# Optimization experiments

Hardware: AMD Instinct MI355X
Metric: run time of the kernel (lower is better)

## Reference

```python
import jax, jax.numpy as jnp
import numpy as np

B, S, E, H = 4, 2048, 1024, 16
D = E // H  # projection_dim = 64


def setup_inputs() -> dict:
    key = jax.random.key(0)
    ks = jax.random.split(key, 6)
    scale = 1.0 / np.sqrt(E)
    return {
        "inputs": jax.random.normal(ks[0], (B, S, E), dtype=jnp.float32),
        "Wq": jax.random.normal(ks[1], (E, E), dtype=jnp.float32) * scale,
        "bq": jnp.zeros((E,), dtype=jnp.float32),
        "Wk": jax.random.normal(ks[2], (E, E), dtype=jnp.float32) * scale,
        "bk": jnp.zeros((E,), dtype=jnp.float32),
        "Wv": jax.random.normal(ks[3], (E, E), dtype=jnp.float32) * scale,
        "bv": jnp.zeros((E,), dtype=jnp.float32),
        "Wo": jax.random.normal(ks[4], (E, E), dtype=jnp.float32) * scale,
        "bo": jnp.zeros((E,), dtype=jnp.float32),
    }


def _split_heads(x):
    # [B,S,E] -> [B,H,S,D]
    b, s, _ = x.shape
    return x.reshape(b, s, H, D).transpose(0, 2, 1, 3)


def reference(inputs, Wq, bq, Wk, bk, Wv, bv, Wo, bo):
    q = _split_heads(inputs @ Wq + bq)
    k = _split_heads(inputs @ Wk + bk)
    v = _split_heads(inputs @ Wv + bv)
    inv_sqrt_d = jnp.float32(1.0) / jnp.sqrt(jnp.float32(D))
    # scores: [B,H,S,S]
    scores = jnp.einsum("bhqd,bhkd->bhqk", q, k) * inv_sqrt_d
    weights = jax.nn.softmax(scores, axis=-1)
    attn = jnp.einsum("bhqk,bhkd->bhqd", weights, v)  # [B,H,S,D]
    attn = attn.transpose(0, 2, 1, 3).reshape(inputs.shape[0], -1, E)  # [B,S,E]
    return attn @ Wo + bo
```

## Files before the change

kernel.cpp:

```cpp
#include <hip/hip_runtime.h>
#include <hip/hip_bf16.h>


#define S_LEN 2048
#define E_DIM 1024
#define H_NUM 16
#define D_DIM 64
#define M_ROWS 8192
#define NT (S_LEN / 64)

typedef float f32x4 __attribute__((ext_vector_type(4)));
typedef __bf16 b16x8 __attribute__((ext_vector_type(8)));
typedef unsigned short u16x8 __attribute__((ext_vector_type(8)));
typedef unsigned short u16x4 __attribute__((ext_vector_type(4)));
typedef unsigned int u32x4 __attribute__((ext_vector_type(4)));

static __device__ __forceinline__ f32x4 mfma_bf16(b16x8 a, b16x8 b, f32x4 c) {
  return __builtin_amdgcn_mfma_f32_16x16x32_bf16(a, b, c, 0, 0, 0);
}

static __device__ __forceinline__ unsigned short f2b(float f) {
  union { float f; unsigned u; } v;
  v.f = f;
  unsigned r = v.u + 0x7fffu + ((v.u >> 16) & 1u);
  return (unsigned short)(r >> 16);
}

static __device__ __forceinline__ unsigned pack_bf16x2(float a, float b) {
  __hip_bfloat162 h2 = __float22bfloat162_rn(make_float2(a, b));
  union { __hip_bfloat162 h; unsigned u; } p;
  p.h = h2;
  return p.u;
}

static __device__ __forceinline__ void async_ld16(const unsigned short* g,
                                                  const unsigned short* lds) {
  __builtin_amdgcn_global_load_lds(
      (const __attribute__((address_space(1))) void*)g,
      (__attribute__((address_space(3))) void*)lds, 16, 0, 0);
}


__global__ __launch_bounds__(256) void f32_to_bf16_kernel(
    const float* __restrict__ in, unsigned short* __restrict__ out, int n4) {
  const int i = blockIdx.x * 256 + threadIdx.x;
  if (i >= n4) return;
  const f32x4 v = *(const f32x4*)&in[(size_t)i * 4];
  u16x4 o;
  o.x = f2b(v.x); o.y = f2b(v.y); o.z = f2b(v.z); o.w = f2b(v.w);
  *(u16x4*)&out[(size_t)i * 4] = o;
}

__global__ __launch_bounds__(256) void transpose_w_kernel(
    const float* __restrict__ in, unsigned short* __restrict__ out) {
  __shared__ float tile[32][33];
  const int bx = blockIdx.x * 32, by = blockIdx.y * 32;
  const int tx = threadIdx.x & 31;
  const int ty = (threadIdx.x >> 5) * 4;
#pragma unroll
  for (int i = 0; i < 4; ++i)
    tile[ty + i][tx] = in[(size_t)(by + ty + i) * 1024 + bx + tx];
  __syncthreads();
#pragma unroll
  for (int i = 0; i < 4; ++i)
    out[(size_t)(bx + ty + i) * 1024 + by + tx] = f2b(tile[tx][ty + i]);
}


template <int OUT_F32>
__global__ __launch_bounds__(256) void gemm_bt_kernel(
    const unsigned short* __restrict__ A, const unsigned short* __restrict__ Bt,
    const float* __restrict__ bias, void* __restrict__ Cout, int M, int N,
    int K, float scale) {
  __shared__ __align__(16) unsigned short As[128 * 32];
  __shared__ __align__(16) unsigned short Bs[128 * 32];

  const int tid = threadIdx.x;
  const int wid = tid >> 6;
  const int l = tid & 63;
  const int g = l >> 4;
  const int c = l & 15;
  const int wm = wid >> 1;
  const int wn = wid & 1;
  const int mbase = blockIdx.x * 128;
  const int nbase = blockIdx.y * 128;
  const int lrow = l >> 2;
  const int scol = (l & 3) * 8;

  f32x4 acc[4][4];
#pragma unroll
  for (int i = 0; i < 4; ++i)
#pragma unroll
    for (int j = 0; j < 4; ++j) acc[i][j] = (f32x4){0.f, 0.f, 0.f, 0.f};

  for (int kt = 0; kt < K; kt += 32) {
#pragma unroll
    for (int i = 0; i < 2; ++i) {
      const int ci = wid * 2 + i;
      const int row = ci * 16 + lrow;
      async_ld16(A + (size_t)(mbase + row) * K + kt + scol, As + ci * 512);
      async_ld16(Bt + (size_t)(nbase + row) * K + kt + scol, Bs + ci * 512);
    }
    __syncthreads();

    b16x8 af[4], bfr[4];
#pragma unroll
    for (int mi = 0; mi < 4; ++mi)
      af[mi] = *(const b16x8*)&As[(wm * 64 + mi * 16 + c) * 32 + g * 8];
#pragma unroll
    for (int ni = 0; ni < 4; ++ni)
      bfr[ni] = *(const b16x8*)&Bs[(wn * 64 + ni * 16 + c) * 32 + g * 8];
#pragma unroll
    for (int mi = 0; mi < 4; ++mi)
#pragma unroll
      for (int ni = 0; ni < 4; ++ni)
        acc[mi][ni] = mfma_bf16(af[mi], bfr[ni], acc[mi][ni]);
    __syncthreads();
  }

#pragma unroll
  for (int ni = 0; ni < 4; ++ni) {
    const int col = nbase + wn * 64 + ni * 16 + c;
    const float bv = bias[col];
#pragma unroll
    for (int mi = 0; mi < 4; ++mi)
#pragma unroll
      for (int r = 0; r < 4; ++r) {
        const int row = mbase + wm * 64 + mi * 16 + g * 4 + r;
        const float v = (acc[mi][ni][r] + bv) * scale;
        if (OUT_F32)
          ((float*)Cout)[(size_t)row * N + col] = v;
        else
          ((unsigned short*)Cout)[(size_t)row * N + col] = f2b(v);
      }
  }
}


__global__ __launch_bounds__(256) void attn_kernel(
    const unsigned short* __restrict__ Q, const unsigned short* __restrict__ K,
    const unsigned short* __restrict__ V, unsigned short* __restrict__ O) {
  __shared__ __align__(16) unsigned short Klds[64 * 72];
  __shared__ __align__(16) unsigned short Vt[64 * 72];

  const int tid = threadIdx.x;
  const int w = tid >> 6;
  const int l = tid & 63;
  const int g = l >> 4;
  const int c = l & 15;
  const int b = blockIdx.y >> 4;
  const int h = blockIdx.y & 15;
  const int qbase = blockIdx.x * 128;
  const size_t base_bh = (size_t)b * S_LEN * E_DIM + h * D_DIM;

  const int srow0 = tid >> 3;
  const int scolc = (tid & 7) * 8;
  const int schunk = scolc >> 3;

  b16x8 qf[2][2];
#pragma unroll
  for (int m = 0; m < 2; ++m)
#pragma unroll
    for (int kk = 0; kk < 2; ++kk) {
      const int row = qbase + w * 32 + m * 16 + c;
      qf[m][kk] = *(const b16x8*)&Q[base_bh + (size_t)row * E_DIM + kk * 32 + g * 8];
    }

  f32x4 o[2][4];
#pragma unroll
  for (int m = 0; m < 2; ++m)
#pragma unroll
    for (int nd = 0; nd < 4; ++nd) o[m][nd] = (f32x4){0.f, 0.f, 0.f, 0.f};
  float mrun[2], lrun[2];
  mrun[0] = mrun[1] = -3.0e38f;
  lrun[0] = lrun[1] = 0.f;

  u16x8 kreg[2], vreg[2];

#define LOAD_TILE(T)                                                        \
  {                                                                         \
    const int kvb_ = (T) * 64;                                              \
    _Pragma("unroll") for (int i = 0; i < 2; ++i) {                         \
      const int row_ = srow0 + i * 32;                                      \
      const size_t ga_ = base_bh + (size_t)(kvb_ + row_) * E_DIM + scolc;   \
      kreg[i] = *(const u16x8*)&K[ga_];                                     \
      vreg[i] = *(const u16x8*)&V[ga_];                                     \
    }                                                                       \
  }
#define WRITE_TILE()                                                        \
  {                                                                         \
    _Pragma("unroll") for (int i = 0; i < 2; ++i) {                         \
      const int row_ = srow0 + i * 32;                                      \
      *(u16x8*)&Klds[row_ * 72 + scolc] = kreg[i];                          \
      const int chunk_ = ((row_ >> 3) ^ schunk) & 7;                        \
      _Pragma("unroll") for (int j = 0; j < 8; ++j)                         \
          Vt[(scolc + j) * 72 + chunk_ * 8 + (row_ & 7)] = vreg[i][j];      \
    }                                                                       \
  }

  LOAD_TILE(0);
  WRITE_TILE();

  const int srcA = (((2 * g) & 3) << 4) + c;
  const int srcB = (((2 * g + 1) & 3) << 4) + c;
  const int fsel = g >> 1;

  for (int t = 0; t < NT; ++t) {
    if (t + 1 < NT) LOAD_TILE(t + 1);
    __syncthreads();

    f32x4 sacc[4][2];
#pragma unroll
    for (int n = 0; n < 4; ++n)
#pragma unroll
      for (int m = 0; m < 2; ++m) sacc[n][m] = (f32x4){0.f, 0.f, 0.f, 0.f};
#pragma unroll
    for (int n = 0; n < 4; ++n)
#pragma unroll
      for (int kk = 0; kk < 2; ++kk) {
        const b16x8 kf = *(const b16x8*)&Klds[(n * 16 + c) * 72 + kk * 32 + g * 8];
#pragma unroll
        for (int m = 0; m < 2; ++m)
          sacc[n][m] = mfma_bf16(kf, qf[m][kk], sacc[n][m]);
      }

#pragma unroll
    for (int m = 0; m < 2; ++m) {
      float mx = sacc[0][m][0];
#pragma unroll
      for (int n = 0; n < 4; ++n)
#pragma unroll
        for (int r = 0; r < 4; ++r) mx = fmaxf(mx, sacc[n][m][r]);
      mx = fmaxf(mx, __shfl_xor(mx, 16));
      mx = fmaxf(mx, __shfl_xor(mx, 32));
      const float mnew = fmaxf(mrun[m], mx);
      const float corr = __expf(mrun[m] - mnew);
      mrun[m] = mnew;
      float ps = 0.f;
#pragma unroll
      for (int n = 0; n < 4; ++n)
#pragma unroll
        for (int r = 0; r < 4; ++r) {
          const float p = __expf(sacc[n][m][r] - mnew);
          sacc[n][m][r] = p;
          ps += p;
        }
      ps += __shfl_xor(ps, 16);
      ps += __shfl_xor(ps, 32);
      lrun[m] = lrun[m] * corr + ps;

#pragma unroll
      for (int r = 0; r < 4; ++r) {
        const float cr = __shfl(corr, g * 20 + r);
#pragma unroll
        for (int nd = 0; nd < 4; ++nd) o[m][nd][r] *= cr;
      }

      unsigned wpk[4][2];
#pragma unroll
      for (int n = 0; n < 4; ++n)
#pragma unroll
        for (int rr = 0; rr < 2; ++rr)
          wpk[n][rr] = pack_bf16x2(sacc[n][m][2 * rr], sacc[n][m][2 * rr + 1]);

#pragma unroll
      for (int kk = 0; kk < 2; ++kk) {
        const unsigned aL0 = (unsigned)__shfl((int)wpk[2 * kk][0], srcA);
        const unsigned aL1 = (unsigned)__shfl((int)wpk[2 * kk][1], srcA);
        const unsigned bL0 = (unsigned)__shfl((int)wpk[2 * kk + 1][0], srcA);
        const unsigned bL1 = (unsigned)__shfl((int)wpk[2 * kk + 1][1], srcA);
        const unsigned aH0 = (unsigned)__shfl((int)wpk[2 * kk][0], srcB);
        const unsigned aH1 = (unsigned)__shfl((int)wpk[2 * kk][1], srcB);
        const unsigned bH0 = (unsigned)__shfl((int)wpk[2 * kk + 1][0], srcB);
        const unsigned bH1 = (unsigned)__shfl((int)wpk[2 * kk + 1][1], srcB);
        union { u32x4 u; b16x8 bv; } pun;
        pun.u = (u32x4){fsel ? bL0 : aL0, fsel ? bL1 : aL1,
                        fsel ? bH0 : aH0, fsel ? bH1 : aH1};
        const b16x8 pf = pun.bv;
#pragma unroll
        for (int nd = 0; nd < 4; ++nd) {
          const int d = nd * 16 + c;
          const int chunk = ((kk * 4 + g) ^ (d >> 3)) & 7;
          const b16x8 vf = *(const b16x8*)&Vt[d * 72 + chunk * 8];
          o[m][nd] = mfma_bf16(pf, vf, o[m][nd]);
        }
      }
    }

    __syncthreads();
    if (t + 1 < NT) WRITE_TILE();
  }

#pragma unroll
  for (int m = 0; m < 2; ++m) {
    const float inv = 1.f / lrun[m];
#pragma unroll
    for (int r = 0; r < 4; ++r) {
      const float ivr = __shfl(inv, g * 20 + r);
      const int row = qbase + w * 32 + m * 16 + g * 4 + r;
#pragma unroll
      for (int nd = 0; nd < 4; ++nd)
        O[base_bh + (size_t)row * E_DIM + nd * 16 + c] = f2b(o[m][nd][r] * ivr);
    }
  }
#undef LOAD_TILE
#undef WRITE_TILE
}


extern "C" void kernel_launch(void* const* d_in, const int* in_sizes, int n_in,
                              void* d_out, int out_size, void* d_ws,
                              size_t ws_size, hipStream_t stream) {
  const float* X = (const float*)d_in[0];
  const float* Wq = (const float*)d_in[1];
  const float* bq = (const float*)d_in[2];
  const float* Wk = (const float*)d_in[3];
  const float* bk = (const float*)d_in[4];
  const float* Wv = (const float*)d_in[5];
  const float* bv = (const float*)d_in[6];
  const float* Wo = (const float*)d_in[7];
  const float* bo = (const float*)d_in[8];
  float* out = (float*)d_out;

  unsigned short* ws = (unsigned short*)d_ws;
  unsigned short* Xb = ws;
  unsigned short* Wqt = Xb + 8388608;
  unsigned short* Wkt = Wqt + 1048576;
  unsigned short* Wvt = Wkt + 1048576;
  unsigned short* Wot = Wvt + 1048576;
  unsigned short* Qb = Wot + 1048576;
  unsigned short* Kb = Qb + 8388608;
  unsigned short* Vb = Kb + 8388608;
  unsigned short* Ab = Xb;

  f32_to_bf16_kernel<<<8192, 256, 0, stream>>>(X, Xb, 2097152);
  dim3 tg(32, 32);
  transpose_w_kernel<<<tg, 256, 0, stream>>>(Wq, Wqt);
  transpose_w_kernel<<<tg, 256, 0, stream>>>(Wk, Wkt);
  transpose_w_kernel<<<tg, 256, 0, stream>>>(Wv, Wvt);
  transpose_w_kernel<<<tg, 256, 0, stream>>>(Wo, Wot);

  dim3 gg(M_ROWS / 128, E_DIM / 128);
  gemm_bt_kernel<0><<<gg, 256, 0, stream>>>(Xb, Wqt, bq, (void*)Qb, M_ROWS,
                                            E_DIM, E_DIM, 0.125f);
  gemm_bt_kernel<0><<<gg, 256, 0, stream>>>(Xb, Wkt, bk, (void*)Kb, M_ROWS,
                                            E_DIM, E_DIM, 1.0f);
  gemm_bt_kernel<0><<<gg, 256, 0, stream>>>(Xb, Wvt, bv, (void*)Vb, M_ROWS,
                                            E_DIM, E_DIM, 1.0f);

  dim3 ga(S_LEN / 128, 4 * H_NUM);
  attn_kernel<<<ga, 256, 0, stream>>>(Qb, Kb, Vb, Ab);

  gemm_bt_kernel<1><<<gg, 256, 0, stream>>>(Ab, Wot, bo, (void*)out, M_ROWS,
                                            E_DIM, E_DIM, 1.0f);
}
```

Baseline: 408.1 us.

## Fuse QKV projections into one GEMM and double-buffer attention K/V tiles

The three Q/K/V projection GEMMs become a single GEMM against the concatenated transposed weights (Wqt/Wkt/Wvt sit contiguously in the workspace), writing an interleaved [M,3072] bf16 buffer that attention reads with stride 3072. This cuts launches and re-reads of X. The attention kernel gets double-buffered K/V LDS tiles, so each iteration needs one barrier instead of two. It also raises wave priority around the MFMA blocks and reorders the P·V loop so each V fragment is shared across both row groups. The price is double the LDS per block and strided QKV reads in attention.

```diff
diff --git a/kernel.cpp b/kernel.cpp
--- a/kernel.cpp
+++ b/kernel.cpp
@@ -8,6 +8,7 @@
 #define D_DIM 64
 #define M_ROWS 8192
 #define NT (S_LEN / 64)
+#define QKV_LD 3072
 
 typedef float f32x4 __attribute__((ext_vector_type(4)));
 typedef __bf16 b16x8 __attribute__((ext_vector_type(8)));
@@ -67,11 +68,10 @@
 }
 
 
-template <int OUT_F32>
-__global__ __launch_bounds__(256) void gemm_bt_kernel(
+__global__ __launch_bounds__(256) void gemm_bt_f32_kernel(
     const unsigned short* __restrict__ A, const unsigned short* __restrict__ Bt,
-    const float* __restrict__ bias, void* __restrict__ Cout, int M, int N,
-    int K, float scale) {
+    const float* __restrict__ bias, float* __restrict__ Cout, int M, int N,
+    int K) {
   __shared__ __align__(16) unsigned short As[128 * 32];
   __shared__ __align__(16) unsigned short Bs[128 * 32];
 
@@ -127,21 +127,83 @@
 #pragma unroll
       for (int r = 0; r < 4; ++r) {
         const int row = mbase + wm * 64 + mi * 16 + g * 4 + r;
-        const float v = (acc[mi][ni][r] + bv) * scale;
-        if (OUT_F32)
-          ((float*)Cout)[(size_t)row * N + col] = v;
-        else
-          ((unsigned short*)Cout)[(size_t)row * N + col] = f2b(v);
+        Cout[(size_t)row * N + col] = acc[mi][ni][r] + bv;
+      }
+  }
+}
+
+__global__ __launch_bounds__(256) void gemm_qkv_kernel(
+    const unsigned short* __restrict__ A, const unsigned short* __restrict__ Bt,
+    const float* __restrict__ bq, const float* __restrict__ bk,
+    const float* __restrict__ bv, unsigned short* __restrict__ Cout) {
+  const int M = M_ROWS, N = QKV_LD, K = E_DIM;
+  __shared__ __align__(16) unsigned short As[128 * 32];
+  __shared__ __align__(16) unsigned short Bs[128 * 32];
+
+  const int tid = threadIdx.x;
+  const int wid = tid >> 6;
+  const int l = tid & 63;
+  const int g = l >> 4;
+  const int c = l & 15;
+  const int wm = wid >> 1;
+  const int wn = wid & 1;
+  const int mbase = blockIdx.x * 128;
+  const int nbase = blockIdx.y * 128;
+  const int lrow = l >> 2;
+  const int scol = (l & 3) * 8;
+
+  f32x4 acc[4][4];
+#pragma unroll
+  for (int i = 0; i < 4; ++i)
+#pragma unroll
+    for (int j = 0; j < 4; ++j) acc[i][j] = (f32x4){0.f, 0.f, 0.f, 0.f};
+
+  for (int kt = 0; kt < K; kt += 32) {
+#pragma unroll
+    for (int i = 0; i < 2; ++i) {
+      const int ci = wid * 2 + i;
+      const int row = ci * 16 + lrow;
+      async_ld16(A + (size_t)(mbase + row) * K + kt + scol, As + ci * 512);
+      async_ld16(Bt + (size_t)(nbase + row) * K + kt + scol, Bs + ci * 512);
+    }
+    __syncthreads();
+
+    b16x8 af[4], bfr[4];
+#pragma unroll
+    for (int mi = 0; mi < 4; ++mi)
+      af[mi] = *(const b16x8*)&As[(wm * 64 + mi * 16 + c) * 32 + g * 8];
+#pragma unroll
+    for (int ni = 0; ni < 4; ++ni)
+      bfr[ni] = *(const b16x8*)&Bs[(wn * 64 + ni * 16 + c) * 32 + g * 8];
+#pragma unroll
+    for (int mi = 0; mi < 4; ++mi)
+#pragma unroll
+      for (int ni = 0; ni < 4; ++ni)
+        acc[mi][ni] = mfma_bf16(af[mi], bfr[ni], acc[mi][ni]);
+    __syncthreads();
+  }
+
+#pragma unroll
+  for (int ni = 0; ni < 4; ++ni) {
+    const int col = nbase + wn * 64 + ni * 16 + c;
+    const float* bp = (col < 1024) ? bq : ((col < 2048) ? bk : bv);
+    const float bvv = bp[col & 1023];
+    const float scale = (col < 1024) ? 0.125f : 1.0f;
+#pragma unroll
+    for (int mi = 0; mi < 4; ++mi)
+#pragma unroll
+      for (int r = 0; r < 4; ++r) {
+        const int row = mbase + wm * 64 + mi * 16 + g * 4 + r;
+        Cout[(size_t)row * N + col] = f2b((acc[mi][ni][r] + bvv) * scale);
       }
   }
 }
 
 
 __global__ __launch_bounds__(256) void attn_kernel(
-    const unsigned short* __restrict__ Q, const unsigned short* __restrict__ K,
-    const unsigned short* __restrict__ V, unsigned short* __restrict__ O) {
-  __shared__ __align__(16) unsigned short Klds[64 * 72];
-  __shared__ __align__(16) unsigned short Vt[64 * 72];
+    const unsigned short* __restrict__ QKV, unsigned short* __restrict__ O) {
+  __shared__ __align__(16) unsigned short Klds[2][64 * 72];
+  __shared__ __align__(16) unsigned short Vt[2][64 * 72];
 
   const int tid = threadIdx.x;
   const int w = tid >> 6;
@@ -151,7 +213,10 @@
   const int b = blockIdx.y >> 4;
   const int h = blockIdx.y & 15;
   const int qbase = blockIdx.x * 128;
-  const size_t base_bh = (size_t)b * S_LEN * E_DIM + h * D_DIM;
+  const size_t base_bh = (size_t)b * S_LEN * QKV_LD + h * D_DIM;
+  const unsigned short* Q = QKV;
+  const unsigned short* K = QKV + 1024;
+  const unsigned short* V = QKV + 2048;
 
   const int srow0 = tid >> 3;
   const int scolc = (tid & 7) * 8;
@@ -163,7 +228,8 @@
 #pragma unroll
     for (int kk = 0; kk < 2; ++kk) {
       const int row = qbase + w * 32 + m * 16 + c;
-      qf[m][kk] = *(const b16x8*)&Q[base_bh + (size_t)row * E_DIM + kk * 32 + g * 8];
+      qf[m][kk] =
+          *(const b16x8*)&Q[base_bh + (size_t)row * QKV_LD + kk * 32 + g * 8];
     }
 
   f32x4 o[2][4];
@@ -177,52 +243,59 @@
 
   u16x8 kreg[2], vreg[2];
 
-#define LOAD_TILE(T)                                                        \
-  {                                                                         \
-    const int kvb_ = (T) * 64;                                              \
-    _Pragma("unroll") for (int i = 0; i < 2; ++i) {                         \
-      const int row_ = srow0 + i * 32;                                      \
-      const size_t ga_ = base_bh + (size_t)(kvb_ + row_) * E_DIM + scolc;   \
-      kreg[i] = *(const u16x8*)&K[ga_];                                     \
-      vreg[i] = *(const u16x8*)&V[ga_];                                     \
-    }                                                                       \
-  }
-#define WRITE_TILE()                                                        \
-  {                                                                         \
-    _Pragma("unroll") for (int i = 0; i < 2; ++i) {                         \
-      const int row_ = srow0 + i * 32;                                      \
-      *(u16x8*)&Klds[row_ * 72 + scolc] = kreg[i];                          \
-      const int chunk_ = ((row_ >> 3) ^ schunk) & 7;                        \
-      _Pragma("unroll") for (int j = 0; j < 8; ++j)                         \
-          Vt[(scolc + j) * 72 + chunk_ * 8 + (row_ & 7)] = vreg[i][j];      \
-    }                                                                       \
+#define LOAD_TILE(T)                                                         \
+  {                                                                          \
+    const int kvb_ = (T) * 64;                                               \
+    _Pragma("unroll") for (int i = 0; i < 2; ++i) {                          \
+      const int row_ = srow0 + i * 32;                                       \
+      const size_t ga_ = base_bh + (size_t)(kvb_ + row_) * QKV_LD + scolc;   \
+      kreg[i] = *(const u16x8*)&K[ga_];                                      \
+      vreg[i] = *(const u16x8*)&V[ga_];                                      \
+    }                                                                        \
+  }
+#define WRITE_TILE(BUF)                                                      \
+  {                                                                          \
+    _Pragma("unroll") for (int i = 0; i < 2; ++i) {                          \
+      const int row_ = srow0 + i * 32;                                       \
+      *(u16x8*)&Klds[BUF][row_ * 72 + scolc] = kreg[i];                      \
+      const int chunk_ = ((row_ >> 3) ^ schunk) & 7;                         \
+      _Pragma("unroll") for (int j = 0; j < 8; ++j)                          \
+          Vt[BUF][(scolc + j) * 72 + chunk_ * 8 + (row_ & 7)] = vreg[i][j];  \
+    }                                                                        \
   }
 
   LOAD_TILE(0);
-  WRITE_TILE();
+  WRITE_TILE(0);
 
   const int srcA = (((2 * g) & 3) << 4) + c;
   const int srcB = (((2 * g + 1) & 3) << 4) + c;
   const int fsel = g >> 1;
 
   for (int t = 0; t < NT; ++t) {
+    const int cur = t & 1;
+    __syncthreads();
+
     if (t + 1 < NT) LOAD_TILE(t + 1);
-    __syncthreads();
 
     f32x4 sacc[4][2];
 #pragma unroll
     for (int n = 0; n < 4; ++n)
 #pragma unroll
       for (int m = 0; m < 2; ++m) sacc[n][m] = (f32x4){0.f, 0.f, 0.f, 0.f};
+    __builtin_amdgcn_s_setprio(1);
 #pragma unroll
     for (int n = 0; n < 4; ++n)
 #pragma unroll
       for (int kk = 0; kk < 2; ++kk) {
-        const b16x8 kf = *(const b16x8*)&Klds[(n * 16 + c) * 72 + kk * 32 + g * 8];
+        const b16x8 kf =
+            *(const b16x8*)&Klds[cur][(n * 16 + c) * 72 + kk * 32 + g * 8];
 #pragma unroll
         for (int m = 0; m < 2; ++m)
           sacc[n][m] = mfma_bf16(kf, qf[m][kk], sacc[n][m]);
       }
+    __builtin_amdgcn_s_setprio(0);
+
+    if (t + 1 < NT) WRITE_TILE(cur ^ 1);
 
 #pragma unroll
     for (int m = 0; m < 2; ++m) {
@@ -248,47 +321,49 @@
       ps += __shfl_xor(ps, 16);
       ps += __shfl_xor(ps, 32);
       lrun[m] = lrun[m] * corr + ps;
-
 #pragma unroll
       for (int r = 0; r < 4; ++r) {
         const float cr = __shfl(corr, g * 20 + r);
 #pragma unroll
         for (int nd = 0; nd < 4; ++nd) o[m][nd][r] *= cr;
       }
-
-      unsigned wpk[4][2];
-#pragma unroll
-      for (int n = 0; n < 4; ++n)
-#pragma unroll
-        for (int rr = 0; rr < 2; ++rr)
-          wpk[n][rr] = pack_bf16x2(sacc[n][m][2 * rr], sacc[n][m][2 * rr + 1]);
-
-#pragma unroll
-      for (int kk = 0; kk < 2; ++kk) {
-        const unsigned aL0 = (unsigned)__shfl((int)wpk[2 * kk][0], srcA);
-        const unsigned aL1 = (unsigned)__shfl((int)wpk[2 * kk][1], srcA);
-        const unsigned bL0 = (unsigned)__shfl((int)wpk[2 * kk + 1][0], srcA);
-        const unsigned bL1 = (unsigned)__shfl((int)wpk[2 * kk + 1][1], srcA);
-        const unsigned aH0 = (unsigned)__shfl((int)wpk[2 * kk][0], srcB);
-        const unsigned aH1 = (unsigned)__shfl((int)wpk[2 * kk][1], srcB);
-        const unsigned bH0 = (unsigned)__shfl((int)wpk[2 * kk + 1][0], srcB);
-        const unsigned bH1 = (unsigned)__shfl((int)wpk[2 * kk + 1][1], srcB);
+    }
+
+#pragma unroll
+    for (int kk = 0; kk < 2; ++kk) {
+      b16x8 pf[2];
+#pragma unroll
+      for (int m = 0; m < 2; ++m) {
+        const unsigned w00 = pack_bf16x2(sacc[2 * kk][m][0], sacc[2 * kk][m][1]);
+        const unsigned w01 = pack_bf16x2(sacc[2 * kk][m][2], sacc[2 * kk][m][3]);
+        const unsigned w10 =
+            pack_bf16x2(sacc[2 * kk + 1][m][0], sacc[2 * kk + 1][m][1]);
+        const unsigned w11 =
+            pack_bf16x2(sacc[2 * kk + 1][m][2], sacc[2 * kk + 1][m][3]);
+        const unsigned aL0 = (unsigned)__shfl((int)w00, srcA);
+        const unsigned aL1 = (unsigned)__shfl((int)w01, srcA);
+        const unsigned bL0 = (unsigned)__shfl((int)w10, srcA);
+        const unsigned bL1 = (unsigned)__shfl((int)w11, srcA);
+        const unsigned aH0 = (unsigned)__shfl((int)w00, srcB);
+        const unsigned aH1 = (unsigned)__shfl((int)w01, srcB);
+        const unsigned bH0 = (unsigned)__shfl((int)w10, srcB);
+        const unsigned bH1 = (unsigned)__shfl((int)w11, srcB);
         union { u32x4 u; b16x8 bv; } pun;
         pun.u = (u32x4){fsel ? bL0 : aL0, fsel ? bL1 : aL1,
                         fsel ? bH0 : aH0, fsel ? bH1 : aH1};
-        const b16x8 pf = pun.bv;
-#pragma unroll
-        for (int nd = 0; nd < 4; ++nd) {
-          const int d = nd * 16 + c;
-          const int chunk = ((kk * 4 + g) ^ (d >> 3)) & 7;
-          const b16x8 vf = *(const b16x8*)&Vt[d * 72 + chunk * 8];
-          o[m][nd] = mfma_bf16(pf, vf, o[m][nd]);
-        }
-      }
-    }
-
-    __syncthreads();
-    if (t + 1 < NT) WRITE_TILE();
+        pf[m] = pun.bv;
+      }
+      __builtin_amdgcn_s_setprio(1);
+#pragma unroll
+      for (int nd = 0; nd < 4; ++nd) {
+        const int d = nd * 16 + c;
+        const int chunk = ((kk * 4 + g) ^ (d >> 3)) & 7;
+        const b16x8 vf = *(const b16x8*)&Vt[cur][d * 72 + chunk * 8];
+        o[0][nd] = mfma_bf16(pf[0], vf, o[0][nd]);
+        o[1][nd] = mfma_bf16(pf[1], vf, o[1][nd]);
+      }
+      __builtin_amdgcn_s_setprio(0);
+    }
   }
 
 #pragma unroll
@@ -298,9 +373,10 @@
     for (int r = 0; r < 4; ++r) {
       const float ivr = __shfl(inv, g * 20 + r);
       const int row = qbase + w * 32 + m * 16 + g * 4 + r;
+      const size_t obase = (size_t)b * S_LEN * E_DIM + h * D_DIM;
 #pragma unroll
       for (int nd = 0; nd < 4; ++nd)
-        O[base_bh + (size_t)row * E_DIM + nd * 16 + c] = f2b(o[m][nd][r] * ivr);
+        O[obase + (size_t)row * E_DIM + nd * 16 + c] = f2b(o[m][nd][r] * ivr);
     }
   }
 #undef LOAD_TILE
@@ -328,9 +404,7 @@
   unsigned short* Wkt = Wqt + 1048576;
   unsigned short* Wvt = Wkt + 1048576;
   unsigned short* Wot = Wvt + 1048576;
-  unsigned short* Qb = Wot + 1048576;
-  unsigned short* Kb = Qb + 8388608;
-  unsigned short* Vb = Kb + 8388608;
+  unsigned short* QKVb = Wot + 1048576;
   unsigned short* Ab = Xb;
 
   f32_to_bf16_kernel<<<8192, 256, 0, stream>>>(X, Xb, 2097152);
@@ -340,17 +414,13 @@
   transpose_w_kernel<<<tg, 256, 0, stream>>>(Wv, Wvt);
   transpose_w_kernel<<<tg, 256, 0, stream>>>(Wo, Wot);
 
+  dim3 gq(M_ROWS / 128, QKV_LD / 128);
+  gemm_qkv_kernel<<<gq, 256, 0, stream>>>(Xb, Wqt, bq, bk, bv, QKVb);
+
+  dim3 ga(S_LEN / 128, 4 * H_NUM);
+  attn_kernel<<<ga, 256, 0, stream>>>(QKVb, Ab);
+
   dim3 gg(M_ROWS / 128, E_DIM / 128);
-  gemm_bt_kernel<0><<<gg, 256, 0, stream>>>(Xb, Wqt, bq, (void*)Qb, M_ROWS,
-                                            E_DIM, E_DIM, 0.125f);
-  gemm_bt_kernel<0><<<gg, 256, 0, stream>>>(Xb, Wkt, bk, (void*)Kb, M_ROWS,
-                                            E_DIM, E_DIM, 1.0f);
-  gemm_bt_kernel<0><<<gg, 256, 0, stream>>>(Xb, Wvt, bv, (void*)Vb, M_ROWS,
-                                            E_DIM, E_DIM, 1.0f);
-
-  dim3 ga(S_LEN / 128, 4 * H_NUM);
-  attn_kernel<<<ga, 256, 0, stream>>>(Qb, Kb, Vb, Ab);
-
-  gemm_bt_kernel<1><<<gg, 256, 0, stream>>>(Ab, Wot, bo, (void*)out, M_ROWS,
-                                            E_DIM, E_DIM, 1.0f);
-}
+  gemm_bt_f32_kernel<<<gg, 256, 0, stream>>>(Ab, Wot, bo, out, M_ROWS, E_DIM,
+                                             E_DIM);
+}
```

Result: faster. 372.8 us (-8.7%).
